# Kernel tuning notes

Hardware: AMD Instinct MI355X
Metric: run time of the kernel (lower is better)

## Reference

```python
import jax, jax.numpy as jnp
import numpy as np

P = 7            # cfg.POOLING_SIZE (= group_size)
N_CLASSES = 21   # PASCAL VOC incl. background
SPATIAL_SCALE = 1.0 / 16.0


def _round_half_up(x):
    # matches C round() for non-negative roi coords (jnp.round is banker's)
    return jnp.floor(x + 0.5)


def psroi_pool(feat, rois, out_dim):
    """Position-sensitive RoI average pooling via integral images.
    feat: [B, out_dim*P*P, H, W]; rois: [N, 5] (batch_idx, x1, y1, x2, y2).
    Returns [N, out_dim, P, P]."""
    B, C, H, W = feat.shape
    # summed-area table, zero-padded: S[b,c,h,w] = sum feat[b,c,:h,:w]
    S = jnp.cumsum(jnp.cumsum(feat, axis=2), axis=3)
    S = jnp.pad(S, ((0, 0), (0, 0), (1, 0), (1, 0)))

    b = rois[:, 0].astype(jnp.int32)
    x1 = _round_half_up(rois[:, 1]) * SPATIAL_SCALE
    y1 = _round_half_up(rois[:, 2]) * SPATIAL_SCALE
    x2 = _round_half_up(rois[:, 3] + 1.0) * SPATIAL_SCALE
    y2 = _round_half_up(rois[:, 4] + 1.0) * SPATIAL_SCALE
    roi_w = jnp.maximum(x2 - x1, 0.1)
    roi_h = jnp.maximum(y2 - y1, 0.1)
    bin_w = roi_w / P
    bin_h = roi_h / P

    g = jnp.arange(P, dtype=feat.dtype)
    hs = jnp.clip(jnp.floor(g[None] * bin_h[:, None] + y1[:, None]), 0, H).astype(jnp.int32)        # [N,P]
    he = jnp.clip(jnp.ceil((g[None] + 1.0) * bin_h[:, None] + y1[:, None]), 0, H).astype(jnp.int32)
    ws = jnp.clip(jnp.floor(g[None] * bin_w[:, None] + x1[:, None]), 0, W).astype(jnp.int32)
    we = jnp.clip(jnp.ceil((g[None] + 1.0) * bin_w[:, None] + x1[:, None]), 0, W).astype(jnp.int32)

    # channel for (ctop, gh, gw) is (ctop*P + gh)*P + gw == arange(C) reshaped
    c = jnp.arange(C, dtype=jnp.int32).reshape(1, out_dim, P, P)
    bi = b[:, None, None, None]
    h0 = hs[:, None, :, None]; h1 = he[:, None, :, None]
    w0 = ws[:, None, None, :]; w1 = we[:, None, None, :]
    # box-sum from integral image -> [N, out_dim, P, P]
    ssum = S[bi, c, h1, w1] - S[bi, c, h0, w1] - S[bi, c, h1, w0] + S[bi, c, h0, w0]

    dh = jnp.maximum(he - hs, 0)[:, None, :, None]
    dw = jnp.maximum(we - ws, 0)[:, None, None, :]
    area = (dh * dw).astype(feat.dtype)
    return jnp.where(area > 0, ssum / jnp.maximum(area, 1.0), 0.0)


def setup_inputs() -> dict:
    key = jax.random.key(0)
    k1, k2, k3, k4, k5 = jax.random.split(key, 5)
    B, Cin, H, W = 4, 2048, 64, 64
    base_feat = jax.random.normal(k1, (B, Cin, H, W), jnp.float32)
    w_conv1 = 0.01 * jax.random.normal(k2, (1024, Cin), jnp.float32)
    w_cls = 0.01 * jax.random.normal(k3, (N_CLASSES * P * P, 1024), jnp.float32)
    w_bbox = 0.001 * jax.random.normal(k4, (4 * N_CLASSES * P * P, 1024), jnp.float32)
    # 300 ROIs per image in image coords (image size = 16*H = 1024)
    n_per = 300
    ka, kb = jax.random.split(k5)
    xy1 = jax.random.uniform(ka, (B * n_per, 2), jnp.float32, 0.0, 900.0)
    wh = jax.random.uniform(kb, (B * n_per, 2), jnp.float32, 16.0, 160.0)
    xy2 = jnp.minimum(xy1 + wh, 1023.0)
    bidx = jnp.repeat(jnp.arange(B, dtype=jnp.float32), n_per)[:, None]
    rois = jnp.concatenate([bidx, xy1[:, 0:1], xy1[:, 1:2], xy2[:, 0:1], xy2[:, 1:2]], axis=1)
    return {"base_feat": base_feat, "rois": rois, "w_conv1": w_conv1, "w_cls": w_cls, "w_bbox": w_bbox}


def reference(base_feat, rois, w_conv1, w_cls, w_bbox):
    B = base_feat.shape[0]
    n_per = rois.shape[0] // B
    # 1x1 conv (no bias) + relu
    x = jax.nn.relu(jnp.einsum('oi,bihw->bohw', w_conv1, base_feat))
    # cls branch: 1x1 conv -> PSRoIPool -> PxP avgpool -> softmax
    cls_feat = jnp.einsum('oi,bihw->bohw', w_cls, x)
    pooled_cls = psroi_pool(cls_feat, rois, N_CLASSES)        # [N, 21, P, P]
    cls_score = pooled_cls.mean(axis=(2, 3))                   # [N, 21]
    cls_prob = jax.nn.softmax(cls_score, axis=1)
    # bbox branch: 1x1 conv -> PSRoIPool -> PxP avgpool
    bbox_feat = jnp.einsum('oi,bihw->bohw', w_bbox, x)
    pooled_loc = psroi_pool(bbox_feat, rois, 4 * N_CLASSES)    # [N, 84, P, P]
    bbox_pred = pooled_loc.mean(axis=(2, 3))                    # [N, 84]
    return cls_prob.reshape(B, n_per, -1), bbox_pred.reshape(B, n_per, -1)
```

## Files before the change

kernel.cpp:

```cpp
#include <hip/hip_runtime.h>
#include <cstdint>


typedef __attribute__((ext_vector_type(8))) short short8;
typedef __attribute__((ext_vector_type(4))) short short4v;
typedef __attribute__((ext_vector_type(4))) float f32x4;

#define OFF_FEATT 0ull
#define OFF_W1    67108864ull
#define OFF_X     71303168ull
#define OFF_WC    104857600ull
#define OFF_DESC  117702656ull
#define OFF_P     0ull

__device__ __forceinline__ unsigned short f2bf(float f) {
  unsigned u = __float_as_uint(f);
  u += 0x7fffu + ((u >> 16) & 1u);
  return (unsigned short)(u >> 16);
}
__device__ __forceinline__ float bf2f(unsigned short h) {
  return __uint_as_float(((unsigned)h) << 16);
}

__device__ __forceinline__ int swz6(int k6, int key) {
  return ((((k6 >> 3) & 7) ^ key) << 3) | (k6 & 7);
}

__device__ __forceinline__ void gload16(const void* g, void* l) {
  __builtin_amdgcn_global_load_lds((const __attribute__((address_space(1))) void*)g,
                                   (__attribute__((address_space(3))) void*)l, 16, 0, 0);
}

__global__ __launch_bounds__(256) void k_prep(const float* __restrict__ w_conv1,
                                              const float* __restrict__ wcls,
                                              const float* __restrict__ wbbox,
                                              const float* __restrict__ rois,
                                              const float* __restrict__ base_feat,
                                              unsigned short* __restrict__ w1b,
                                              unsigned short* __restrict__ Wc,
                                              int* __restrict__ desc,
                                              unsigned short* __restrict__ featT) {
  __shared__ float tile[64][65];
  int bid = blockIdx.x;
  if (bid < 2048) {
    int t = bid * 256 + threadIdx.x;
    long e = (long)t * 4;
    int o = (int)(e >> 11), k = (int)(e & 2047);
    float4 q = *(const float4*)(w_conv1 + e);
    short4v s = {(short)f2bf(q.x), (short)f2bf(q.y), (short)f2bf(q.z), (short)f2bf(q.w)};
    int kp = (k & ~63) | swz6(k & 63, o & 7);
    *(short4v*)(w1b + (size_t)o * 2048 + kp) = s;
  } else if (bid < 8320) {
    int t = (bid - 2048) * 256 + threadIdx.x;
    size_t e = (size_t)t * 4;
    int c = (int)(e / 50176);
    int rem = (int)(e - (size_t)c * 50176);
    int ij = rem >> 10, k = rem & 1023;
    float4 q = make_float4(0.f, 0.f, 0.f, 0.f);
    if (c < 21)       q = *(const float4*)(wcls + (size_t)(c * 49 + ij) * 1024 + k);
    else if (c < 105) q = *(const float4*)(wbbox + (size_t)((c - 21) * 49 + ij) * 1024 + k);
    short4v s = {(short)f2bf(q.x), (short)f2bf(q.y), (short)f2bf(q.z), (short)f2bf(q.w)};
    int kp = (k & ~63) | swz6(k & 63, c & 7);
    *(short4v*)(Wc + ((size_t)(c * 49 + ij) * 1024 + kp)) = s;
  } else if (bid < 8565) {
    int t = (bid - 8320) * 256 + threadIdx.x;
    if (t >= 1280 * 49) return;
    int roi = t / 49, ij = t - roi * 49;
    int* d = desc + (size_t)t * 8;
    if (roi >= 1200) { d[0] = 0; d[1] = 0; d[2] = 0; d[3] = 0; d[4] = 0; ((float*)d)[5] = 0.f; return; }
    const float* r = rois + (size_t)roi * 5;
    int b = (int)r[0];
    float x1 = __fmul_rn(floorf(__fadd_rn(r[1], 0.5f)), 0.0625f);
    float y1 = __fmul_rn(floorf(__fadd_rn(r[2], 0.5f)), 0.0625f);
    float x2 = __fmul_rn(floorf(__fadd_rn(__fadd_rn(r[3], 1.0f), 0.5f)), 0.0625f);
    float y2 = __fmul_rn(floorf(__fadd_rn(__fadd_rn(r[4], 1.0f), 0.5f)), 0.0625f);
    float bw = __fdiv_rn(fmaxf(__fsub_rn(x2, x1), 0.1f), 7.0f);
    float bh = __fdiv_rn(fmaxf(__fsub_rn(y2, y1), 0.1f), 7.0f);
    int i = ij / 7, j = ij - (ij / 7) * 7;
    float fi = (float)i, fj = (float)j;
    int hs = (int)fminf(fmaxf(floorf(__fadd_rn(__fmul_rn(fi, bh), y1)), 0.f), 64.f);
    int he = (int)fminf(fmaxf(ceilf(__fadd_rn(__fmul_rn(__fadd_rn(fi, 1.f), bh), y1)), 0.f), 64.f);
    int wsx = (int)fminf(fmaxf(floorf(__fadd_rn(__fmul_rn(fj, bw), x1)), 0.f), 64.f);
    int we = (int)fminf(fmaxf(ceilf(__fadd_rn(__fmul_rn(__fadd_rn(fj, 1.f), bw), x1)), 0.f), 64.f);
    int dh = max(he - hs, 0), dw = max(we - wsx, 0);
    float inv = (dh * dw > 0) ? 1.0f / (float)(dh * dw) : 0.f;
    d[0] = b; d[1] = hs; d[2] = he; d[3] = wsx; d[4] = we;
    ((float*)d)[5] = inv;
  } else {
    int t = bid - 8565;
    int s0 = (t & 63) * 64;
    int c0 = ((t >> 6) & 31) * 64;
    int b = t >> 11;
    int tx4 = (threadIdx.x & 15) * 4;
    int cl0 = threadIdx.x >> 4;
    const float* sp = base_feat + ((size_t)b * 2048 + c0) * 4096 + s0;
#pragma unroll
    for (int i = 0; i < 4; i++) {
      int cl = i * 16 + cl0;
      float4 q = *(const float4*)(sp + (size_t)cl * 4096 + tx4);
      *(float4*)&tile[cl][tx4] = q;
    }
    __syncthreads();
    unsigned short* dp = featT + ((size_t)b * 4096 + s0) * 2048 + c0;
    int c8 = (threadIdx.x & 7) * 8;
    int sy = threadIdx.x >> 3;
#pragma unroll
    for (int i = 0; i < 2; i++) {
      int sl = i * 32 + sy;
      int key = sl & 7;
      short8 v = {(short)f2bf(tile[c8 + 0][sl]), (short)f2bf(tile[c8 + 1][sl]),
                  (short)f2bf(tile[c8 + 2][sl]), (short)f2bf(tile[c8 + 3][sl]),
                  (short)f2bf(tile[c8 + 4][sl]), (short)f2bf(tile[c8 + 5][sl]),
                  (short)f2bf(tile[c8 + 6][sl]), (short)f2bf(tile[c8 + 7][sl])};
      *(short8*)(dp + (size_t)sl * 2048 + ((((c8 >> 3) ^ key) << 3))) = v;
    }
  }
}

__global__ __launch_bounds__(512, 2) void k_gemm_conv1(const short* __restrict__ A,
                                                       const short* __restrict__ Bw,
                                                       unsigned short* __restrict__ X) {
  __shared__ short lds[9 * 8192];
  int mt = blockIdx.x, nt = blockIdx.y;
  int tid = threadIdx.x, lane = tid & 63, wave = tid >> 6;
  int wm = wave >> 2, wn = wave & 3;

  const short* Ab = A + (size_t)mt * 256 * 2048;
  const short* Bb = Bw + (size_t)nt * 256 * 2048;

  f32x4 acc[8][4];
#pragma unroll
  for (int i = 0; i < 8; i++)
#pragma unroll
    for (int j = 0; j < 4; j++) acc[i][j] = (f32x4){0.f, 0.f, 0.f, 0.f};

  int sr = tid >> 3;
  int sc = (tid & 7) * 8;
  auto stage_half = [&](int h) {
    if (h >= 128) return;
    int kind = h & 3, tl = h >> 2, slot = h % 9;
    const short* src = ((kind & 2) ? Bb : Ab)
                     + (size_t)((kind & 1) * 128 + sr) * 2048 + tl * 64 + sc;
    char* dst = (char*)lds + slot * 16384 + tid * 16;
    gload16(src, dst);
    gload16(src + (size_t)64 * 2048, dst + 8192);
  };

#pragma unroll
  for (int h = 0; h < 5; h++) stage_half(h);

  int la15 = lane & 15;
  int key = lane & 7;
  int ko0 = (((lane >> 4)) ^ key) << 3;
  int ko1 = ((4 | (lane >> 4)) ^ key) << 3;
  int bro = (wn & 1) * 64;

  for (int t = 0; t < 32; ++t) {
    if (t < 31) asm volatile("s_waitcnt vmcnt(2)" ::: "memory");
    else        asm volatile("s_waitcnt vmcnt(0)" ::: "memory");
    __builtin_amdgcn_s_barrier();
    __builtin_amdgcn_sched_barrier(0);
    const short* Asl = lds + (size_t)((4 * t + wm) % 9) * 8192;
    const short* Bsl = lds + (size_t)((4 * t + 2 + (wn >> 1)) % 9) * 8192;
    short8 af[4], bf[4];

    stage_half(4 * t + 5);
#pragma unroll
    for (int j = 0; j < 4; j++)
      bf[j] = *(const short8*)(Bsl + (bro + j * 16 + la15) * 64 + ko0);
#pragma unroll
    for (int i = 0; i < 4; i++)
      af[i] = *(const short8*)(Asl + (i * 16 + la15) * 64 + ko0);
    __builtin_amdgcn_s_setprio(1);
#pragma unroll
    for (int i = 0; i < 4; i++)
#pragma unroll
      for (int j = 0; j < 4; j++)
        acc[i][j] = __builtin_amdgcn_mfma_f32_16x16x32_bf16(af[i], bf[j], acc[i][j], 0, 0, 0);
    __builtin_amdgcn_s_setprio(0);

    stage_half(4 * t + 6);
#pragma unroll
    for (int i = 0; i < 4; i++)
      af[i] = *(const short8*)(Asl + (64 + i * 16 + la15) * 64 + ko0);
    __builtin_amdgcn_s_setprio(1);
#pragma unroll
    for (int i = 0; i < 4; i++)
#pragma unroll
      for (int j = 0; j < 4; j++)
        acc[4 + i][j] = __builtin_amdgcn_mfma_f32_16x16x32_bf16(af[i], bf[j], acc[4 + i][j], 0, 0, 0);
    __builtin_amdgcn_s_setprio(0);

    stage_half(4 * t + 7);
#pragma unroll
    for (int j = 0; j < 4; j++)
      bf[j] = *(const short8*)(Bsl + (bro + j * 16 + la15) * 64 + ko1);
#pragma unroll
    for (int i = 0; i < 4; i++)
      af[i] = *(const short8*)(Asl + (i * 16 + la15) * 64 + ko1);
    __builtin_amdgcn_s_setprio(1);
#pragma unroll
    for (int i = 0; i < 4; i++)
#pragma unroll
      for (int j = 0; j < 4; j++)
        acc[i][j] = __builtin_amdgcn_mfma_f32_16x16x32_bf16(af[i], bf[j], acc[i][j], 0, 0, 0);
    __builtin_amdgcn_s_setprio(0);

    stage_half(4 * t + 8);
#pragma unroll
    for (int i = 0; i < 4; i++)
      af[i] = *(const short8*)(Asl + (64 + i * 16 + la15) * 64 + ko1);
    __builtin_amdgcn_s_setprio(1);
#pragma unroll
    for (int i = 0; i < 4; i++)
#pragma unroll
      for (int j = 0; j < 4; j++)
        acc[4 + i][j] = __builtin_amdgcn_mfma_f32_16x16x32_bf16(af[i], bf[j], acc[4 + i][j], 0, 0, 0);
    __builtin_amdgcn_s_setprio(0);
  }

  unsigned short* Xo = X + ((size_t)(mt * 256 + wm * 128)) * 1024 + nt * 256 + wn * 64;
#pragma unroll
  for (int ii = 0; ii < 8; ii++)
#pragma unroll
    for (int j = 0; j < 4; j++) {
      int row = ii * 16 + (lane >> 4) * 4;
      int col = j * 16 + la15;
#pragma unroll
      for (int r = 0; r < 4; r++)
        Xo[(size_t)(row + r) * 1024 + col] = f2bf(fmaxf(acc[ii][j][r], 0.f));
    }
}

__global__ __launch_bounds__(256) void k_fusedpool(const unsigned short* __restrict__ Xb,
                                                   const int* __restrict__ desc,
                                                   const unsigned short* __restrict__ Wc,
                                                   unsigned short* __restrict__ P,
                                                   int nroi) {
  int mt = blockIdx.x;
  int ij = blockIdx.y;
  int kh = blockIdx.z;
  __shared__ short As[64 * 64];
  __shared__ short Bs[128 * 64];
  __shared__ int dsc[64][4];
  int tid = threadIdx.x, lane = tid & 63, wave = tid >> 6;

  if (tid < 64) {
    const int* d = desc + ((size_t)(mt * 64 + tid) * 49 + ij) * 8;
    int b = d[0], hs = d[1], he = d[2], wsx = d[3], we = d[4];
    dsc[tid][0] = (b * 64 + hs) * 64 + wsx;
    dsc[tid][1] = max(he - hs, 0);
    dsc[tid][2] = max(we - wsx, 0);
    dsc[tid][3] = d[5];
  }
  __syncthreads();

  f32x4 acc[4][2];
#pragma unroll
  for (int i = 0; i < 4; i++)
#pragma unroll
    for (int j = 0; j < 2; j++) acc[i][j] = (f32x4){0.f, 0.f, 0.f, 0.f};

  const unsigned short* Bb = Wc + (size_t)ij * 1024;
  int lr = lane >> 3, lc = (lane & 7) * 8;
  int key = lane & 7;
  int r8 = tid >> 3;
  int k8 = tid & 7;

  int kbeg = kh * 512, kend = kbeg + 512;
  for (int k0 = kbeg; k0 < kend; k0 += 64) {
#pragma unroll
    for (int i = 0; i < 4; i++) {
      int row = i * 32 + wave * 8 + lr;
      gload16(Bb + (size_t)row * (49 * 1024) + k0 + lc, (char*)Bs + (i * 32 + wave * 8) * 128);
    }
#pragma unroll 1
    for (int p = 0; p < 2; p++) {
      int r = p * 32 + r8;
      int cs = dsc[r][0], dh = dsc[r][1], dw = dsc[r][2];
      float inv = __int_as_float(dsc[r][3]);
      const unsigned short* xp = Xb + (size_t)cs * 1024 + k0 + k8 * 8;
      float a0 = 0.f, a1 = 0.f, a2 = 0.f, a3 = 0.f;
      float a4 = 0.f, a5 = 0.f, a6 = 0.f, a7 = 0.f;
#pragma unroll
      for (int hh = 0; hh < 3; hh++) {
#pragma unroll
        for (int ww = 0; ww < 3; ww++) {
          int ho = (hh < dh) ? hh : 0;
          int wo = (ww < dw) ? ww : 0;
          float m = ((hh < dh) && (ww < dw)) ? inv : 0.f;
          short8 v = *(const short8*)(xp + (size_t)(ho * 64 + wo) * 1024);
          a0 = fmaf(m, bf2f((unsigned short)v[0]), a0);
          a1 = fmaf(m, bf2f((unsigned short)v[1]), a1);
          a2 = fmaf(m, bf2f((unsigned short)v[2]), a2);
          a3 = fmaf(m, bf2f((unsigned short)v[3]), a3);
          a4 = fmaf(m, bf2f((unsigned short)v[4]), a4);
          a5 = fmaf(m, bf2f((unsigned short)v[5]), a5);
          a6 = fmaf(m, bf2f((unsigned short)v[6]), a6);
          a7 = fmaf(m, bf2f((unsigned short)v[7]), a7);
        }
      }
      short8 o = {(short)f2bf(a0), (short)f2bf(a1), (short)f2bf(a2), (short)f2bf(a3),
                  (short)f2bf(a4), (short)f2bf(a5), (short)f2bf(a6), (short)f2bf(a7)};
      *(short8*)(As + r * 64 + ((k8 ^ (r & 7)) << 3)) = o;
    }
    __syncthreads();
#pragma unroll
    for (int kt = 0; kt < 2; kt++) {
      int ko = (((kt << 2) | (lane >> 4)) ^ key) << 3;
      short8 af[4], bfr[2];
#pragma unroll
      for (int i = 0; i < 4; i++)
        af[i] = *(const short8*)(As + (i * 16 + (lane & 15)) * 64 + ko);
#pragma unroll
      for (int j = 0; j < 2; j++)
        bfr[j] = *(const short8*)(Bs + (wave * 32 + j * 16 + (lane & 15)) * 64 + ko);
#pragma unroll
      for (int i = 0; i < 4; i++)
#pragma unroll
        for (int j = 0; j < 2; j++)
          acc[i][j] = __builtin_amdgcn_mfma_f32_16x16x32_bf16(af[i], bfr[j], acc[i][j], 0, 0, 0);
    }
    __syncthreads();
  }
  unsigned short* Pb = P + (size_t)(kh * 49 + ij) * nroi * 112;
#pragma unroll
  for (int i = 0; i < 4; i++)
#pragma unroll
    for (int j = 0; j < 2; j++) {
      int cc = wave * 32 + j * 16 + (lane & 15);
      if (cc < 112) {
        int rbase = mt * 64 + i * 16 + (lane >> 4) * 4;
#pragma unroll
        for (int r = 0; r < 4; r++)
          Pb[(size_t)(rbase + r) * 112 + cc] = f2bf(acc[i][j][r]);
      }
    }
}

__global__ __launch_bounds__(128) void k_redfinal(const unsigned short* __restrict__ P,
                                                  float* __restrict__ out, int nroi) {
  int roi = blockIdx.x;
  int c = threadIdx.x;
  __shared__ float sc[112];
  __shared__ float es[32];
  if (c < 112) {
    const unsigned short* p = P + (size_t)roi * 112 + c;
    float s = 0.f;
#pragma unroll 7
    for (int ij = 0; ij < 98; ij++) s += bf2f(p[(size_t)ij * nroi * 112]);
    sc[c] = s * (1.f / 49.f);
  }
  __syncthreads();
  if (c < 21) {
    float mx = -1e30f;
#pragma unroll
    for (int k = 0; k < 21; k++) mx = fmaxf(mx, sc[k]);
    es[c] = expf(sc[c] - mx);
  }
  __syncthreads();
  if (c < 21) {
    float sum = 0.f;
#pragma unroll
    for (int k = 0; k < 21; k++) sum += es[k];
    float rs = 1.f / sum;
    out[(size_t)roi * 21 + c] = es[c] * rs;
  }
  if (c >= 21 && c < 105) {
    out[25200 + (size_t)roi * 84 + (c - 21)] = sc[c];
  }
}

extern "C" void kernel_launch(void* const* d_in, const int* in_sizes, int n_in,
                              void* d_out, int out_size, void* d_ws, size_t ws_size,
                              hipStream_t stream) {
  const float* base_feat = (const float*)d_in[0];
  const float* rois      = (const float*)d_in[1];
  const float* w_conv1   = (const float*)d_in[2];
  const float* w_cls     = (const float*)d_in[3];
  const float* w_bbox    = (const float*)d_in[4];
  float* out = (float*)d_out;
  char* ws = (char*)d_ws;

  unsigned short* featT = (unsigned short*)(ws + OFF_FEATT);
  unsigned short* w1b   = (unsigned short*)(ws + OFF_W1);
  unsigned short* X     = (unsigned short*)(ws + OFF_X);
  unsigned short* Wc    = (unsigned short*)(ws + OFF_WC);
  int*            desc  = (int*)(ws + OFF_DESC);
  unsigned short* P     = (unsigned short*)(ws + OFF_P);

  k_prep<<<16757, 256, 0, stream>>>(w_conv1, w_cls, w_bbox, rois, base_feat,
                                    w1b, Wc, desc, featT);
  k_gemm_conv1<<<dim3(64, 4), 512, 0, stream>>>((const short*)featT, (const short*)w1b, X);
  k_fusedpool<<<dim3(20, 49, 2), 256, 0, stream>>>(X, desc, Wc, P, 1280);
  k_redfinal<<<1200, 128, 0, stream>>>(P, out, 1280);
}
```

Baseline: 358.5 us.

## Double transpose tile per block and widen fused pool kernel to 512 threads

The transpose part of the prep kernel now handles two 64-spatial tiles per block, issuing all eight float4 loads before the LDS writes, and the grid is shrunk to match. The fused pool kernel moves to 512 threads, so each thread gathers one ROI row instead of looping over two. All nine bf16 neighbour vectors are loaded up front to expose memory-level parallelism, and each wave owns one 16-column MFMA tile. The intent is more latency hiding on the gather-bound pooling and fewer prep blocks, at the cost of higher register pressure and LDS use.

```diff
diff --git a/kernel.cpp b/kernel.cpp
--- a/kernel.cpp
+++ b/kernel.cpp
@@ -40,7 +40,7 @@
                                               unsigned short* __restrict__ Wc,
                                               int* __restrict__ desc,
                                               unsigned short* __restrict__ featT) {
-  __shared__ float tile[64][65];
+  __shared__ float tile2[2][64][65];
   int bid = blockIdx.x;
   if (bid < 2048) {
     int t = bid * 256 + threadIdx.x;
@@ -88,31 +88,41 @@
     ((float*)d)[5] = inv;
   } else {
     int t = bid - 8565;
-    int s0 = (t & 63) * 64;
-    int c0 = ((t >> 6) & 31) * 64;
-    int b = t >> 11;
+    int s0 = (t & 31) * 128;
+    int c0 = ((t >> 5) & 31) * 64;
+    int b = t >> 10;
     int tx4 = (threadIdx.x & 15) * 4;
     int cl0 = threadIdx.x >> 4;
     const float* sp = base_feat + ((size_t)b * 2048 + c0) * 4096 + s0;
-#pragma unroll
-    for (int i = 0; i < 4; i++) {
-      int cl = i * 16 + cl0;
-      float4 q = *(const float4*)(sp + (size_t)cl * 4096 + tx4);
-      *(float4*)&tile[cl][tx4] = q;
-    }
+    float4 q[8];
+#pragma unroll
+    for (int tt = 0; tt < 2; tt++)
+#pragma unroll
+      for (int i = 0; i < 4; i++) {
+        int cl = i * 16 + cl0;
+        q[tt * 4 + i] = *(const float4*)(sp + (size_t)cl * 4096 + tt * 64 + tx4);
+      }
+#pragma unroll
+    for (int tt = 0; tt < 2; tt++)
+#pragma unroll
+      for (int i = 0; i < 4; i++)
+        *(float4*)&tile2[tt][i * 16 + cl0][tx4] = q[tt * 4 + i];
     __syncthreads();
-    unsigned short* dp = featT + ((size_t)b * 4096 + s0) * 2048 + c0;
     int c8 = (threadIdx.x & 7) * 8;
     int sy = threadIdx.x >> 3;
 #pragma unroll
-    for (int i = 0; i < 2; i++) {
-      int sl = i * 32 + sy;
-      int key = sl & 7;
-      short8 v = {(short)f2bf(tile[c8 + 0][sl]), (short)f2bf(tile[c8 + 1][sl]),
-                  (short)f2bf(tile[c8 + 2][sl]), (short)f2bf(tile[c8 + 3][sl]),
-                  (short)f2bf(tile[c8 + 4][sl]), (short)f2bf(tile[c8 + 5][sl]),
-                  (short)f2bf(tile[c8 + 6][sl]), (short)f2bf(tile[c8 + 7][sl])};
-      *(short8*)(dp + (size_t)sl * 2048 + ((((c8 >> 3) ^ key) << 3))) = v;
+    for (int tt = 0; tt < 2; tt++) {
+      unsigned short* dp = featT + ((size_t)b * 4096 + s0 + tt * 64) * 2048 + c0;
+#pragma unroll
+      for (int i = 0; i < 2; i++) {
+        int sl = i * 32 + sy;
+        int key = sl & 7;
+        short8 v = {(short)f2bf(tile2[tt][c8 + 0][sl]), (short)f2bf(tile2[tt][c8 + 1][sl]),
+                    (short)f2bf(tile2[tt][c8 + 2][sl]), (short)f2bf(tile2[tt][c8 + 3][sl]),
+                    (short)f2bf(tile2[tt][c8 + 4][sl]), (short)f2bf(tile2[tt][c8 + 5][sl]),
+                    (short)f2bf(tile2[tt][c8 + 6][sl]), (short)f2bf(tile2[tt][c8 + 7][sl])};
+        *(short8*)(dp + (size_t)sl * 2048 + ((((c8 >> 3) ^ key) << 3))) = v;
+      }
     }
   }
 }
@@ -232,7 +242,7 @@
     }
 }
 
-__global__ __launch_bounds__(256) void k_fusedpool(const unsigned short* __restrict__ Xb,
+__global__ __launch_bounds__(512) void k_fusedpool(const unsigned short* __restrict__ Xb,
                                                    const int* __restrict__ desc,
                                                    const unsigned short* __restrict__ Wc,
                                                    unsigned short* __restrict__ P,
@@ -255,87 +265,83 @@
   }
   __syncthreads();
 
-  f32x4 acc[4][2];
-#pragma unroll
-  for (int i = 0; i < 4; i++)
-#pragma unroll
-    for (int j = 0; j < 2; j++) acc[i][j] = (f32x4){0.f, 0.f, 0.f, 0.f};
+  f32x4 acc[4];
+#pragma unroll
+  for (int i = 0; i < 4; i++) acc[i] = (f32x4){0.f, 0.f, 0.f, 0.f};
 
   const unsigned short* Bb = Wc + (size_t)ij * 1024;
   int lr = lane >> 3, lc = (lane & 7) * 8;
   int key = lane & 7;
-  int r8 = tid >> 3;
+  int la15 = lane & 15;
+  int r64 = tid >> 3;
   int k8 = tid & 7;
+  int cs = dsc[r64][0], dh = dsc[r64][1], dw = dsc[r64][2];
+  float inv = __int_as_float(dsc[r64][3]);
+  int aswz = r64 * 64 + ((k8 ^ (r64 & 7)) << 3);
 
   int kbeg = kh * 512, kend = kbeg + 512;
   for (int k0 = kbeg; k0 < kend; k0 += 64) {
-#pragma unroll
-    for (int i = 0; i < 4; i++) {
-      int row = i * 32 + wave * 8 + lr;
-      gload16(Bb + (size_t)row * (49 * 1024) + k0 + lc, (char*)Bs + (i * 32 + wave * 8) * 128);
+    const unsigned short* xp = Xb + (size_t)cs * 1024 + k0 + k8 * 8;
+    short8 v[9];
+#pragma unroll
+    for (int hh = 0; hh < 3; hh++)
+#pragma unroll
+      for (int ww = 0; ww < 3; ww++) {
+        int ho = (hh < dh) ? hh : 0;
+        int wo = (ww < dw) ? ww : 0;
+        v[hh * 3 + ww] = *(const short8*)(xp + (size_t)(ho * 64 + wo) * 1024);
+      }
+    {
+      int row = wave * 8 + lr;
+      gload16(Bb + (size_t)row * (49 * 1024) + k0 + lc, (char*)Bs + wave * 1024);
+      gload16(Bb + (size_t)(row + 64) * (49 * 1024) + k0 + lc, (char*)Bs + 8192 + wave * 1024);
     }
-#pragma unroll 1
-    for (int p = 0; p < 2; p++) {
-      int r = p * 32 + r8;
-      int cs = dsc[r][0], dh = dsc[r][1], dw = dsc[r][2];
-      float inv = __int_as_float(dsc[r][3]);
-      const unsigned short* xp = Xb + (size_t)cs * 1024 + k0 + k8 * 8;
-      float a0 = 0.f, a1 = 0.f, a2 = 0.f, a3 = 0.f;
-      float a4 = 0.f, a5 = 0.f, a6 = 0.f, a7 = 0.f;
-#pragma unroll
-      for (int hh = 0; hh < 3; hh++) {
-#pragma unroll
-        for (int ww = 0; ww < 3; ww++) {
-          int ho = (hh < dh) ? hh : 0;
-          int wo = (ww < dw) ? ww : 0;
-          float m = ((hh < dh) && (ww < dw)) ? inv : 0.f;
-          short8 v = *(const short8*)(xp + (size_t)(ho * 64 + wo) * 1024);
-          a0 = fmaf(m, bf2f((unsigned short)v[0]), a0);
-          a1 = fmaf(m, bf2f((unsigned short)v[1]), a1);
-          a2 = fmaf(m, bf2f((unsigned short)v[2]), a2);
-          a3 = fmaf(m, bf2f((unsigned short)v[3]), a3);
-          a4 = fmaf(m, bf2f((unsigned short)v[4]), a4);
-          a5 = fmaf(m, bf2f((unsigned short)v[5]), a5);
-          a6 = fmaf(m, bf2f((unsigned short)v[6]), a6);
-          a7 = fmaf(m, bf2f((unsigned short)v[7]), a7);
-        }
+    float a0 = 0.f, a1 = 0.f, a2 = 0.f, a3 = 0.f;
+    float a4 = 0.f, a5 = 0.f, a6 = 0.f, a7 = 0.f;
+#pragma unroll
+    for (int hh = 0; hh < 3; hh++)
+#pragma unroll
+      for (int ww = 0; ww < 3; ww++) {
+        float m = ((hh < dh) && (ww < dw)) ? inv : 0.f;
+        short8 vv = v[hh * 3 + ww];
+        a0 = fmaf(m, bf2f((unsigned short)vv[0]), a0);
+        a1 = fmaf(m, bf2f((unsigned short)vv[1]), a1);
+        a2 = fmaf(m, bf2f((unsigned short)vv[2]), a2);
+        a3 = fmaf(m, bf2f((unsigned short)vv[3]), a3);
+        a4 = fmaf(m, bf2f((unsigned short)vv[4]), a4);
+        a5 = fmaf(m, bf2f((unsigned short)vv[5]), a5);
+        a6 = fmaf(m, bf2f((unsigned short)vv[6]), a6);
+        a7 = fmaf(m, bf2f((unsigned short)vv[7]), a7);
       }
-      short8 o = {(short)f2bf(a0), (short)f2bf(a1), (short)f2bf(a2), (short)f2bf(a3),
-                  (short)f2bf(a4), (short)f2bf(a5), (short)f2bf(a6), (short)f2bf(a7)};
-      *(short8*)(As + r * 64 + ((k8 ^ (r & 7)) << 3)) = o;
+    short8 o = {(short)f2bf(a0), (short)f2bf(a1), (short)f2bf(a2), (short)f2bf(a3),
+                (short)f2bf(a4), (short)f2bf(a5), (short)f2bf(a6), (short)f2bf(a7)};
+    *(short8*)(As + aswz) = o;
+    __syncthreads();
+#pragma unroll
+    for (int kt = 0; kt < 2; kt++) {
+      int ko = (((kt << 2) | (lane >> 4)) ^ key) << 3;
+      short8 bfr = *(const short8*)(Bs + (wave * 16 + la15) * 64 + ko);
+      short8 af[4];
+#pragma unroll
+      for (int i = 0; i < 4; i++)
+        af[i] = *(const short8*)(As + (i * 16 + la15) * 64 + ko);
+#pragma unroll
+      for (int i = 0; i < 4; i++)
+        acc[i] = __builtin_amdgcn_mfma_f32_16x16x32_bf16(af[i], bfr, acc[i], 0, 0, 0);
     }
     __syncthreads();
-#pragma unroll
-    for (int kt = 0; kt < 2; kt++) {
-      int ko = (((kt << 2) | (lane >> 4)) ^ key) << 3;
-      short8 af[4], bfr[2];
-#pragma unroll
-      for (int i = 0; i < 4; i++)
-        af[i] = *(const short8*)(As + (i * 16 + (lane & 15)) * 64 + ko);
-#pragma unroll
-      for (int j = 0; j < 2; j++)
-        bfr[j] = *(const short8*)(Bs + (wave * 32 + j * 16 + (lane & 15)) * 64 + ko);
-#pragma unroll
-      for (int i = 0; i < 4; i++)
-#pragma unroll
-        for (int j = 0; j < 2; j++)
-          acc[i][j] = __builtin_amdgcn_mfma_f32_16x16x32_bf16(af[i], bfr[j], acc[i][j], 0, 0, 0);
+  }
+  unsigned short* Pb = P + (size_t)(kh * 49 + ij) * nroi * 112;
+  int cc = wave * 16 + la15;
+  if (cc < 112) {
+#pragma unroll
+    for (int i = 0; i < 4; i++) {
+      int rbase = mt * 64 + i * 16 + (lane >> 4) * 4;
+#pragma unroll
+      for (int r = 0; r < 4; r++)
+        Pb[(size_t)(rbase + r) * 112 + cc] = f2bf(acc[i][r]);
     }
-    __syncthreads();
-  }
-  unsigned short* Pb = P + (size_t)(kh * 49 + ij) * nroi * 112;
-#pragma unroll
-  for (int i = 0; i < 4; i++)
-#pragma unroll
-    for (int j = 0; j < 2; j++) {
-      int cc = wave * 32 + j * 16 + (lane & 15);
-      if (cc < 112) {
-        int rbase = mt * 64 + i * 16 + (lane >> 4) * 4;
-#pragma unroll
-        for (int r = 0; r < 4; r++)
-          Pb[(size_t)(rbase + r) * 112 + cc] = f2bf(acc[i][j][r]);
-      }
-    }
+  }
 }
 
 __global__ __launch_bounds__(128) void k_redfinal(const unsigned short* __restrict__ P,
@@ -389,9 +395,9 @@
   int*            desc  = (int*)(ws + OFF_DESC);
   unsigned short* P     = (unsigned short*)(ws + OFF_P);
 
-  k_prep<<<16757, 256, 0, stream>>>(w_conv1, w_cls, w_bbox, rois, base_feat,
+  k_prep<<<12661, 256, 0, stream>>>(w_conv1, w_cls, w_bbox, rois, base_feat,
                                     w1b, Wc, desc, featT);
   k_gemm_conv1<<<dim3(64, 4), 512, 0, stream>>>((const short*)featT, (const short*)w1b, X);
-  k_fusedpool<<<dim3(20, 49, 2), 256, 0, stream>>>(X, desc, Wc, P, 1280);
+  k_fusedpool<<<dim3(20, 49, 2), 512, 0, stream>>>(X, desc, Wc, P, 1280);
   k_redfinal<<<1200, 128, 0, stream>>>(P, out, 1280);
 }
```

After: 356.1 us. No clear change (-0.7%).
